# Kernel optimization log

Measured on AMD Instinct MI355X. Metric: run time of the kernel, lower is better.

The kernel has to match this reference:

```python
import jax, jax.numpy as jnp
import numpy as np
from jax import lax

B, C, W, H = 4, 64, 128, 128
K = 9            # snake kernel length
OC = 64          # out channels
EXTEND_SCOPE = 1.0
EPS = 1e-5
DN = ('NCHW', 'OIHW', 'NCHW')


def setup_inputs() -> dict:
    key = jax.random.key(0)
    ks = jax.random.split(key, 4)
    f = jax.random.normal(ks[0], (B, C, W, H), jnp.float32)
    offset_w = jax.random.normal(ks[1], (2 * K, C, 3, 3), jnp.float32) * 0.05
    offset_b = jnp.zeros((2 * K,), jnp.float32)
    bn_gamma = jnp.ones((2 * K,), jnp.float32)
    bn_beta = jnp.zeros((2 * K,), jnp.float32)
    bn_mean = jnp.zeros((2 * K,), jnp.float32)
    bn_var = jnp.ones((2 * K,), jnp.float32)
    conv_w = jax.random.normal(ks[2], (OC, C, K, 1), jnp.float32) * 0.05
    conv_b = jnp.zeros((OC,), jnp.float32)
    gn_gamma = jnp.ones((OC,), jnp.float32)
    gn_beta = jnp.zeros((OC,), jnp.float32)
    return dict(f=f, offset_w=offset_w, offset_b=offset_b, bn_gamma=bn_gamma,
                bn_beta=bn_beta, bn_mean=bn_mean, bn_var=bn_var,
                conv_w=conv_w, conv_b=conv_b, gn_gamma=gn_gamma, gn_beta=gn_beta)


def _dsconv(f, offset_w, offset_b, bn_gamma, bn_beta, bn_mean, bn_var,
            conv_w, conv_b, gn_gamma, gn_beta):
    # 1) offset branch: 3x3 conv -> BN (eval) -> tanh
    off = lax.conv_general_dilated(f, offset_w, (1, 1), 'SAME', dimension_numbers=DN)
    off = off + offset_b[None, :, None, None]
    off = (off - bn_mean[None, :, None, None]) * lax.rsqrt(bn_var + EPS)[None, :, None, None]
    off = off * bn_gamma[None, :, None, None] + bn_beta[None, :, None, None]
    off = jnp.tanh(off)
    y_off = off[:, :K]                      # [B,K,W,H]  (morph==0 uses y offsets)

    # 2) cumulative offset recurrence outward from the kernel center.
    # NOTE: indices 0 and K-1 keep their raw (non-accumulated) offsets,
    # exactly reproducing the original loop `for i in range(1, center)`.
    c = K // 2
    offs = [y_off[:, k] for k in range(K)]  # each [B,W,H]
    new = list(offs)
    new[c] = jnp.zeros_like(offs[c])
    for i in range(1, c):
        new[c + i] = new[c + i - 1] + offs[c + i]
        new[c - i] = new[c - i + 1] + offs[c - i]
    y_cum = jnp.stack(new, axis=1)          # [B,K,W,H]

    # 3) sampling coordinates (morph==0): y = row index + accumulated offset,
    # x = col index + linspace(-K//2, K//2, K) (python floor-div semantics).
    lin = jnp.linspace((-K) // 2, K // 2, K).astype(f.dtype)      # [-5..4] for K=9
    y = jnp.arange(W, dtype=f.dtype)[None, None, :, None] + y_cum * EXTEND_SCOPE
    x = jnp.broadcast_to(jnp.arange(H, dtype=f.dtype)[None, None, None, :]
                         + lin[None, :, None, None], (B, K, W, H))
    # layout [B, K*W, H] with row index = w*K + k
    ys = jnp.transpose(y, (0, 2, 1, 3)).reshape(B, K * W, H)
    xs = jnp.transpose(x, (0, 2, 1, 3)).reshape(B, K * W, H)

    # 4) bilinear gather from f (NCHW -> BWHC for channel-last gathers)
    y0 = jnp.clip(jnp.floor(ys).astype(jnp.int32), 0, W - 1)
    y1 = jnp.clip(y0 + 1, 0, W - 1)
    x0 = jnp.clip(jnp.floor(xs).astype(jnp.int32), 0, H - 1)
    x1 = jnp.clip(x0 + 1, 0, H - 1)
    fb = jnp.transpose(f, (0, 2, 3, 1))                  # [B,W,H,C]
    gather = jax.vmap(lambda fm, yy, xx: fm[yy, xx])     # -> [B,K*W,H,C]
    va0 = gather(fb, y0, x0)
    va1 = gather(fb, y0, x1)
    vb0 = gather(fb, y1, x0)
    vb1 = gather(fb, y1, x1)
    y0f, y1f = y0.astype(f.dtype), y1.astype(f.dtype)
    x0f, x1f = x0.astype(f.dtype), x1.astype(f.dtype)
    out = (va0 * ((y1f - ys) * (x1f - xs))[..., None]
           + va1 * ((y1f - ys) * (xs - x0f))[..., None]
           + vb0 * ((ys - y0f) * (x1f - xs))[..., None]
           + vb1 * ((ys - y0f) * (xs - x0f))[..., None])
    deformed = jnp.transpose(out, (0, 3, 1, 2))          # [B,C,K*W,H]

    # 5) (K,1)-strided conv collapses the K snake samples -> [B,OC,W,H]
    z = lax.conv_general_dilated(deformed, conv_w, (K, 1), 'VALID', dimension_numbers=DN)
    z = z + conv_b[None, :, None, None]

    # 6) GroupNorm(OC//4 groups) + ReLU
    G = OC // 4
    zg = z.reshape(B, G, OC // G, W, H)
    mu = zg.mean(axis=(2, 3, 4), keepdims=True)
    var = zg.var(axis=(2, 3, 4), keepdims=True)
    zg = (zg - mu) * lax.rsqrt(var + EPS)
    z = zg.reshape(B, OC, W, H) * gn_gamma[None, :, None, None] + gn_beta[None, :, None, None]
    return jax.nn.relu(z)


def reference(f, offset_w, offset_b, bn_gamma, bn_beta, bn_mean, bn_var,
              conv_w, conv_b, gn_gamma, gn_beta):
    return _dsconv(f, offset_w, offset_b, bn_gamma, bn_beta, bn_mean, bn_var,
                   conv_w, conv_b, gn_gamma, gn_beta)
```

## Files before the change

kernel.cpp:

```cpp
#include <hip/hip_runtime.h>
#include <hip/hip_bf16.h>

#define EPSV 1e-5f

typedef __attribute__((ext_vector_type(8))) short short8;
typedef __attribute__((ext_vector_type(4))) float f32x4;

__device__ __forceinline__ uint2 bilerp_pack(uint2 u00, uint2 u01, uint2 u10, uint2 u11, float4 tw) {
    float a0 = __uint_as_float(u00.x << 16) * tw.x + __uint_as_float(u01.x << 16) * tw.y
             + __uint_as_float(u10.x << 16) * tw.z + __uint_as_float(u11.x << 16) * tw.w;
    float a1 = __uint_as_float(u00.x & 0xffff0000u) * tw.x + __uint_as_float(u01.x & 0xffff0000u) * tw.y
             + __uint_as_float(u10.x & 0xffff0000u) * tw.z + __uint_as_float(u11.x & 0xffff0000u) * tw.w;
    float a2 = __uint_as_float(u00.y << 16) * tw.x + __uint_as_float(u01.y << 16) * tw.y
             + __uint_as_float(u10.y << 16) * tw.z + __uint_as_float(u11.y << 16) * tw.w;
    float a3 = __uint_as_float(u00.y & 0xffff0000u) * tw.x + __uint_as_float(u01.y & 0xffff0000u) * tw.y
             + __uint_as_float(u10.y & 0xffff0000u) * tw.z + __uint_as_float(u11.y & 0xffff0000u) * tw.w;
    uint2 pk;
    pk.x = (uint)__bfloat16_as_ushort(__float2bfloat16(a0))
         | ((uint)__bfloat16_as_ushort(__float2bfloat16(a1)) << 16);
    pk.y = (uint)__bfloat16_as_ushort(__float2bfloat16(a2))
         | ((uint)__bfloat16_as_ushort(__float2bfloat16(a3)) << 16);
    return pk;
}

__global__ __launch_bounds__(256) void k_pre(const float* __restrict__ f,
                                             const float* __restrict__ cw,
                                             const float* __restrict__ ow,
                                             ushort* __restrict__ fbh,
                                             ushort* __restrict__ flo,
                                             ushort* __restrict__ wpk,
                                             ushort* __restrict__ wpk2,
                                             float* __restrict__ stats) {
    int blk = blockIdx.x;
    int t = threadIdx.x;
    if (blk < 1024) {
        __shared__ float tile[64][65];
        int xt = blk & 1;
        int y  = (blk >> 1) & 127;
        int b  = blk >> 8;
        int x = t & 63, c0 = t >> 6;
        const float* src = f + (((size_t)b * 64) * 128 + y) * 128 + xt * 64;
#pragma unroll
        for (int i = 0; i < 64; i += 4)
            tile[c0 + i][x] = src[(size_t)(c0 + i) * 16384 + x];
        __syncthreads();
        size_t dbase = (((size_t)b * 128 + y) * 128 + xt * 64) * 64;
        int cc = t & 63, x0 = t >> 6;
#pragma unroll
        for (int i = 0; i < 64; i += 4) {
            float v = tile[cc][x0 + i];
            ushort hi = __bfloat16_as_ushort(__float2bfloat16(v));
            float vhi = __uint_as_float((uint)hi << 16);
            ushort lo = __bfloat16_as_ushort(__float2bfloat16(v - vhi));
            fbh[dbase + (size_t)(x0 + i) * 64 + cc] = hi;
            flo[dbase + (size_t)(x0 + i) * 64 + cc] = lo;
        }
    } else if (blk < 1168) {
        int idx = (blk - 1024) * 256 + t;
        int j  = idx & 7;
        int l  = (idx >> 3) & 63;
        int ot = (idx >> 9) & 3;
        int kk = (idx >> 11) & 1;
        int k  = idx >> 12;
        int c  = kk * 32 + ((l >> 4) << 3) + j;
        int oc = (ot << 4) + (l & 15);
        wpk[idx] = __bfloat16_as_ushort(__float2bfloat16(cw[((size_t)oc * 64 + c) * 9 + k]));
        if (idx < 128) stats[idx] = 0.f;
    } else {
        int idx = (blk - 1168) * 256 + t;
        int j   = idx & 7;
        int l   = (idx >> 3) & 63;
        int kk  = (idx >> 9) & 1;
        int tap = idx >> 10;
        int c   = kk * 32 + ((l >> 4) << 3) + j;
        int n   = l & 15;
        float v = (n < 9) ? ow[((size_t)n * 64 + c) * 9 + tap] : 0.f;
        ushort hi = __bfloat16_as_ushort(__float2bfloat16(v));
        float vhi = __uint_as_float((uint)hi << 16);
        ushort lo = __bfloat16_as_ushort(__float2bfloat16(v - vhi));
        wpk2[idx] = hi;
        wpk2[idx + 9216] = lo;
    }
}

__global__ __launch_bounds__(256) void k_fused(
    const ushort* __restrict__ fbh,
    const ushort* __restrict__ flo,
    const ushort* __restrict__ wpk,
    const ushort* __restrict__ wpk2,
    const float* __restrict__ ob, const float* __restrict__ bng,
    const float* __restrict__ bnb, const float* __restrict__ bnm,
    const float* __restrict__ bnv, const float* __restrict__ cb,
    float* __restrict__ z, float* __restrict__ stats)
{
    __shared__ struct {
        ushort AH[2][2048];
        ushort AL[2][2048];
        float  tup[9][32][8];
        float  cs[32][12];
    } smx;
    __shared__ float redS[16], redQ[16];

    int jb = blockIdx.x;
    int orig = (jb & 7) * 256 + (jb >> 3);
    int hq = orig & 3;
    int w  = (orig >> 2) & 127;
    int b  = orig >> 9;
    int t    = threadIdx.x;
    int lane = t & 63;
    int wid  = t >> 6;
    int m = wid & 1;
    int n = wid >> 1;

    const char* fpH = (const char*)fbh;
    const char* fpL = (const char*)flo;
    int cg  = t & 15;
    int pq  = t >> 4;
    int cgo = cg << 3;

    int frow = (m << 4) + (lane & 15);
    int frb0 = (frow << 7) + (((lane >> 4) << 4) ^ ((lane & 7) << 4));

    f32x4 acc0k = {0.f, 0.f, 0.f, 0.f};
    const short8* wp2 = (const short8*)wpk2;

    {
        int ysrc = w - 1;
        bool rok = (unsigned)ysrc < 128u;
        char* AbH = (char*)smx.AH[0];
        char* AbL = (char*)smx.AL[0];
#pragma unroll
        for (int s = 0; s < 2; ++s) {
            int px = pq + (s << 4);
            int xsrc = (hq << 5) + px - 1;
            uint2 vh = make_uint2(0u, 0u), vl = make_uint2(0u, 0u);
            if (rok && ((unsigned)xsrc < 128u)) {
                int off = ((((((b << 7) + ysrc) << 7) + xsrc)) << 7) + cgo;
                vh = *(const uint2*)(fpH + off);
                vl = *(const uint2*)(fpL + off);
            }
            int wb = (px << 7) + (cgo ^ ((px & 7) << 4));
            *(uint2*)(AbH + wb) = vh;
            *(uint2*)(AbL + wb) = vl;
        }
    }
    for (int tap = 0; tap < 9; ++tap) {
        __syncthreads();
        int cur = tap & 1;
        uint2 gh[2] = {make_uint2(0u, 0u), make_uint2(0u, 0u)};
        uint2 gl[2] = {make_uint2(0u, 0u), make_uint2(0u, 0u)};
        if (tap < 8) {
            int tn = tap + 1;
            int dy = tn / 3;
            int dx = tn - dy * 3;
            int ysrc = w + dy - 1;
            bool rok = (unsigned)ysrc < 128u;
#pragma unroll
            for (int s = 0; s < 2; ++s) {
                int px = pq + (s << 4);
                int xsrc = (hq << 5) + px + dx - 1;
                if (rok && ((unsigned)xsrc < 128u)) {
                    int off = ((((((b << 7) + ysrc) << 7) + xsrc)) << 7) + cgo;
                    gh[s] = *(const uint2*)(fpH + off);
                    gl[s] = *(const uint2*)(fpL + off);
                }
            }
        }
        if (wid < 2) {
            const char* ArH = (const char*)smx.AH[cur];
            const char* ArL = (const char*)smx.AL[cur];
            short8 ah0 = *(const short8*)(ArH + frb0);
            short8 ah1 = *(const short8*)(ArH + (frb0 ^ 64));
            short8 al0 = *(const short8*)(ArL + frb0);
            short8 al1 = *(const short8*)(ArL + (frb0 ^ 64));
            short8 wh0 = wp2[(tap * 2 + 0) * 64 + lane];
            short8 wh1 = wp2[(tap * 2 + 1) * 64 + lane];
            short8 wl0 = wp2[1152 + (tap * 2 + 0) * 64 + lane];
            short8 wl1 = wp2[1152 + (tap * 2 + 1) * 64 + lane];
            acc0k = __builtin_amdgcn_mfma_f32_16x16x32_bf16(ah0, wh0, acc0k, 0, 0, 0);
            acc0k = __builtin_amdgcn_mfma_f32_16x16x32_bf16(al0, wh0, acc0k, 0, 0, 0);
            acc0k = __builtin_amdgcn_mfma_f32_16x16x32_bf16(ah0, wl0, acc0k, 0, 0, 0);
            acc0k = __builtin_amdgcn_mfma_f32_16x16x32_bf16(ah1, wh1, acc0k, 0, 0, 0);
            acc0k = __builtin_amdgcn_mfma_f32_16x16x32_bf16(al1, wh1, acc0k, 0, 0, 0);
            acc0k = __builtin_amdgcn_mfma_f32_16x16x32_bf16(ah1, wl1, acc0k, 0, 0, 0);
        }
        if (tap < 8) {
            char* AbH = (char*)smx.AH[cur ^ 1];
            char* AbL = (char*)smx.AL[cur ^ 1];
#pragma unroll
            for (int s = 0; s < 2; ++s) {
                int px = pq + (s << 4);
                int wb = (px << 7) + (cgo ^ ((px & 7) << 4));
                *(uint2*)(AbH + wb) = gh[s];
                *(uint2*)(AbL + wb) = gl[s];
            }
        }
    }
    if (wid < 2) {
#pragma unroll
        for (int r = 0; r < 4; ++r) {
            int pxo = (m << 4) + ((lane >> 4) << 2) + r;
            int ko = lane & 15;
            if (ko < 9) smx.cs[pxo][ko] = acc0k[r];
        }
    }
    __syncthreads();
    if (t < 32) {
        float tk[9];
#pragma unroll
        for (int k = 0; k < 9; ++k) {
            float zz = smx.cs[t][k] + ob[k];
            zz = (zz - bnm[k]) * rsqrtf(bnv[k] + EPSV);
            zz = zz * bng[k] + bnb[k];
            tk[k] = tanhf(zz);
        }
        float nw_[9];
        nw_[4] = 0.f;
        nw_[5] = tk[5];
        nw_[6] = nw_[5] + tk[6];
        nw_[7] = nw_[6] + tk[7];
        nw_[8] = tk[8];
        nw_[3] = tk[3];
        nw_[2] = nw_[3] + tk[2];
        nw_[1] = nw_[2] + tk[1];
        nw_[0] = tk[0];
        int h = (hq << 5) + t;
#pragma unroll
        for (int k = 0; k < 9; ++k) {
            float ys = (float)w + nw_[k];
            float xs = (float)h + (-5.0f + 1.125f * (float)k);
            int y0 = min(max((int)floorf(ys), 0), 127);
            int y1 = min(y0 + 1, 127);
            int x0 = min(max((int)floorf(xs), 0), 127);
            int x1 = min(x0 + 1, 127);
            float wy0 = (float)y1 - ys, wy1 = ys - (float)y0;
            float wx0 = (float)x1 - xs, wx1 = xs - (float)x0;
            float* tp = smx.tup[k][t];
            tp[0] = __int_as_float(((((b << 7) + y0) << 7) + x0) << 7);
            tp[1] = __int_as_float(((((b << 7) + y0) << 7) + x1) << 7);
            tp[2] = __int_as_float(((((b << 7) + y1) << 7) + x0) << 7);
            tp[3] = __int_as_float(((((b << 7) + y1) << 7) + x1) << 7);
            tp[4] = wy0 * wx0;
            tp[5] = wy0 * wx1;
            tp[6] = wy1 * wx0;
            tp[7] = wy1 * wx1;
        }
    }
    __syncthreads();

    f32x4 acc0 = {0.f, 0.f, 0.f, 0.f};
    f32x4 acc1 = {0.f, 0.f, 0.f, 0.f};
    const short8* wp8 = (const short8*)wpk;

    {
        char* Ab = (char*)smx.AH[0];
#pragma unroll
        for (int s = 0; s < 2; ++s) {
            int px = pq + (s << 4);
            const float* tp = smx.tup[0][px];
            float4 tr = *(const float4*)tp;
            float4 tw = *(const float4*)(tp + 4);
            uint2 u00 = *(const uint2*)(fpH + __float_as_int(tr.x) + cgo);
            uint2 u01 = *(const uint2*)(fpH + __float_as_int(tr.y) + cgo);
            uint2 u10 = *(const uint2*)(fpH + __float_as_int(tr.z) + cgo);
            uint2 u11 = *(const uint2*)(fpH + __float_as_int(tr.w) + cgo);
            *(uint2*)(Ab + (px << 7) + (cgo ^ ((px & 7) << 4))) = bilerp_pack(u00, u01, u10, u11, tw);
        }
    }
    for (int k = 0; k < 9; ++k) {
        __syncthreads();
        int cur = k & 1;
        uint2 u[2][4];
        float4 twn[2];
        if (k < 8) {
#pragma unroll
            for (int s = 0; s < 2; ++s) {
                int px = pq + (s << 4);
                const float* tp = smx.tup[k + 1][px];
                float4 tr = *(const float4*)tp;
                twn[s] = *(const float4*)(tp + 4);
                u[s][0] = *(const uint2*)(fpH + __float_as_int(tr.x) + cgo);
                u[s][1] = *(const uint2*)(fpH + __float_as_int(tr.y) + cgo);
                u[s][2] = *(const uint2*)(fpH + __float_as_int(tr.z) + cgo);
                u[s][3] = *(const uint2*)(fpH + __float_as_int(tr.w) + cgo);
            }
        }
        int fb0 = (k * 8 + (n << 1)) * 64 + lane;
        short8 wf00 = wp8[fb0];
        short8 wf01 = wp8[fb0 + 64];
        short8 wf10 = wp8[fb0 + 256];
        short8 wf11 = wp8[fb0 + 320];
        const char* Ar = (const char*)smx.AH[cur];
        short8 af0 = *(const short8*)(Ar + frb0);
        short8 af1 = *(const short8*)(Ar + (frb0 ^ 64));
        acc0 = __builtin_amdgcn_mfma_f32_16x16x32_bf16(af0, wf00, acc0, 0, 0, 0);
        acc0 = __builtin_amdgcn_mfma_f32_16x16x32_bf16(af1, wf10, acc0, 0, 0, 0);
        acc1 = __builtin_amdgcn_mfma_f32_16x16x32_bf16(af0, wf01, acc1, 0, 0, 0);
        acc1 = __builtin_amdgcn_mfma_f32_16x16x32_bf16(af1, wf11, acc1, 0, 0, 0);
        if (k < 8) {
            char* Ab = (char*)smx.AH[cur ^ 1];
#pragma unroll
            for (int s = 0; s < 2; ++s) {
                int px = pq + (s << 4);
                *(uint2*)(Ab + (px << 7) + (cgo ^ ((px & 7) << 4))) =
                    bilerp_pack(u[s][0], u[s][1], u[s][2], u[s][3], twn[s]);
            }
        }
    }

    float* Z2 = (float*)&smx;
    int lane15 = lane & 15;
    float b0 = cb[(n << 5) + lane15];
    float b1 = cb[(n << 5) + 16 + lane15];
    float v00 = acc0.x + b0, v01 = acc0.y + b0, v02 = acc0.z + b0, v03 = acc0.w + b0;
    float v10 = acc1.x + b1, v11 = acc1.y + b1, v12 = acc1.z + b1, v13 = acc1.w + b1;
    float s0 = v00 + v01 + v02 + v03;
    float q0 = v00 * v00 + v01 * v01 + v02 * v02 + v03 * v03;
    float s1 = v10 + v11 + v12 + v13;
    float q1 = v10 * v10 + v11 * v11 + v12 * v12 + v13 * v13;
    if (t < 16) { redS[t] = 0.f; redQ[t] = 0.f; }
    __syncthreads();
    int g0 = (n << 3) + (lane15 >> 2);
    atomicAdd(&redS[g0], s0);     atomicAdd(&redQ[g0], q0);
    atomicAdd(&redS[g0 + 4], s1); atomicAdd(&redQ[g0 + 4], q1);
    int pxb = (m << 4) + ((lane >> 4) << 2);
    int ocb = (n << 5) + lane15;
    Z2[(pxb + 0) * 65 + ocb] = v00;
    Z2[(pxb + 1) * 65 + ocb] = v01;
    Z2[(pxb + 2) * 65 + ocb] = v02;
    Z2[(pxb + 3) * 65 + ocb] = v03;
    Z2[(pxb + 0) * 65 + ocb + 16] = v10;
    Z2[(pxb + 1) * 65 + ocb + 16] = v11;
    Z2[(pxb + 2) * 65 + ocb + 16] = v12;
    Z2[(pxb + 3) * 65 + ocb + 16] = v13;
    __syncthreads();
    if (t < 16) {
        atomicAdd(&stats[((size_t)b * 16 + t) * 2 + 0], redS[t]);
        atomicAdd(&stats[((size_t)b * 16 + t) * 2 + 1], redQ[t]);
    }
    int oc = t >> 2, part = t & 3;
    float4 o0, o1;
    o0.x = Z2[(part * 8 + 0) * 65 + oc];
    o0.y = Z2[(part * 8 + 1) * 65 + oc];
    o0.z = Z2[(part * 8 + 2) * 65 + oc];
    o0.w = Z2[(part * 8 + 3) * 65 + oc];
    o1.x = Z2[(part * 8 + 4) * 65 + oc];
    o1.y = Z2[(part * 8 + 5) * 65 + oc];
    o1.z = Z2[(part * 8 + 6) * 65 + oc];
    o1.w = Z2[(part * 8 + 7) * 65 + oc];
    float* zp = z + (((size_t)(b << 6) + oc) << 14) + (w << 7) + (hq << 5) + part * 8;
    *(float4*)zp = o0;
    *(float4*)(zp + 4) = o1;
}

__global__ __launch_bounds__(256) void k_gn(const float* __restrict__ z,
                                            const float* __restrict__ stats,
                                            const float* __restrict__ gg,
                                            const float* __restrict__ gb,
                                            float* __restrict__ out) {
    int idx = blockIdx.x * 256 + threadIdx.x;
    size_t base = (size_t)idx * 4;
    int oc = (int)((base >> 14) & 63);
    int b  = (int)(base >> 20);
    int g  = oc >> 2;
    float sm = stats[((size_t)b * 16 + g) * 2 + 0];
    float sq = stats[((size_t)b * 16 + g) * 2 + 1];
    const float cnt = 65536.f;
    float mu  = sm / cnt;
    float var = sq / cnt - mu * mu;
    float inv = rsqrtf(var + EPSV);
    float gam = gg[oc] * inv;
    float bet = gb[oc] - mu * gam;
    float4 v = *(const float4*)(z + base);
    v.x = fmaxf(v.x * gam + bet, 0.f);
    v.y = fmaxf(v.y * gam + bet, 0.f);
    v.z = fmaxf(v.z * gam + bet, 0.f);
    v.w = fmaxf(v.w * gam + bet, 0.f);
    *(float4*)(out + base) = v;
}

extern "C" void kernel_launch(void* const* d_in, const int* in_sizes, int n_in,
                              void* d_out, int out_size, void* d_ws, size_t ws_size,
                              hipStream_t stream) {
    const float* f   = (const float*)d_in[0];
    const float* ow  = (const float*)d_in[1];
    const float* ob  = (const float*)d_in[2];
    const float* bng = (const float*)d_in[3];
    const float* bnb = (const float*)d_in[4];
    const float* bnm = (const float*)d_in[5];
    const float* bnv = (const float*)d_in[6];
    const float* cw  = (const float*)d_in[7];
    const float* cb  = (const float*)d_in[8];
    const float* gg  = (const float*)d_in[9];
    const float* gb  = (const float*)d_in[10];

    char* wsb = (char*)d_ws;
    ushort* fbh  = (ushort*)wsb;
    ushort* flo  = (ushort*)(wsb + 8388608);
    ushort* wpk  = (ushort*)(wsb + 16777216);
    ushort* wpk2 = (ushort*)(wsb + 16850944);
    float*  z    = (float*)(wsb + 16887808);
    float*  st   = (float*)(wsb + 33665024);

    k_pre<<<1204, 256, 0, stream>>>(f, cw, ow, fbh, flo, wpk, wpk2, st);
    k_fused<<<2048, 256, 0, stream>>>(fbh, flo, wpk, wpk2, ob, bng, bnb, bnm, bnv, cb, z, st);
    k_gn<<<4096, 256, 0, stream>>>(z, st, gg, gb, (float*)d_out);
}
```

Baseline: 158.2 us.

## Stage a 9-row bf16 input window in LDS via direct global-to-LDS loads

The fused kernel now preloads a 9-row by 42-column bf16 window of the input for each block into shared memory using global_load_lds, overlapping the load with the offset-conv MFMA pass. The deformable bilinear samples are then gathered from LDS instead of global memory, and the per-tap double-buffered staging loops with their barriers are removed. The intermediate z tensor is also stored as bf16, with k_gn reading eight values per thread, which halves the intermediate traffic at some precision cost. This trades a much larger LDS footprint for fewer scattered global gathers, and occupancy is capped at three blocks per CU.

```diff
diff --git a/kernel.cpp b/kernel.cpp
--- a/kernel.cpp
+++ b/kernel.cpp
@@ -6,21 +6,26 @@
 typedef __attribute__((ext_vector_type(8))) short short8;
 typedef __attribute__((ext_vector_type(4))) float f32x4;
 
-__device__ __forceinline__ uint2 bilerp_pack(uint2 u00, uint2 u01, uint2 u10, uint2 u11, float4 tw) {
-    float a0 = __uint_as_float(u00.x << 16) * tw.x + __uint_as_float(u01.x << 16) * tw.y
-             + __uint_as_float(u10.x << 16) * tw.z + __uint_as_float(u11.x << 16) * tw.w;
-    float a1 = __uint_as_float(u00.x & 0xffff0000u) * tw.x + __uint_as_float(u01.x & 0xffff0000u) * tw.y
-             + __uint_as_float(u10.x & 0xffff0000u) * tw.z + __uint_as_float(u11.x & 0xffff0000u) * tw.w;
-    float a2 = __uint_as_float(u00.y << 16) * tw.x + __uint_as_float(u01.y << 16) * tw.y
-             + __uint_as_float(u10.y << 16) * tw.z + __uint_as_float(u11.y << 16) * tw.w;
-    float a3 = __uint_as_float(u00.y & 0xffff0000u) * tw.x + __uint_as_float(u01.y & 0xffff0000u) * tw.y
-             + __uint_as_float(u10.y & 0xffff0000u) * tw.z + __uint_as_float(u11.y & 0xffff0000u) * tw.w;
-    uint2 pk;
-    pk.x = (uint)__bfloat16_as_ushort(__float2bfloat16(a0))
-         | ((uint)__bfloat16_as_ushort(__float2bfloat16(a1)) << 16);
-    pk.y = (uint)__bfloat16_as_ushort(__float2bfloat16(a2))
-         | ((uint)__bfloat16_as_ushort(__float2bfloat16(a3)) << 16);
-    return pk;
+__device__ __forceinline__ void gl_lds16(const void* g, void* l) {
+    __builtin_amdgcn_global_load_lds(
+        (const __attribute__((address_space(1))) unsigned int*)g,
+        (__attribute__((address_space(3))) unsigned int*)l, 16, 0, 0);
+}
+
+__device__ __forceinline__ unsigned int bl2(unsigned int a, unsigned int b,
+                                            unsigned int c, unsigned int d,
+                                            float w00, float w01, float w10, float w11) {
+    float lo = __uint_as_float(a << 16) * w00 + __uint_as_float(b << 16) * w01
+             + __uint_as_float(c << 16) * w10 + __uint_as_float(d << 16) * w11;
+    float hi = __uint_as_float(a & 0xffff0000u) * w00 + __uint_as_float(b & 0xffff0000u) * w01
+             + __uint_as_float(c & 0xffff0000u) * w10 + __uint_as_float(d & 0xffff0000u) * w11;
+    return ((unsigned int)__bfloat16_as_ushort(__float2bfloat16(lo)))
+         | (((unsigned int)__bfloat16_as_ushort(__float2bfloat16(hi))) << 16);
+}
+
+__device__ __forceinline__ unsigned int pk2(float a, float b) {
+    return ((unsigned int)__bfloat16_as_ushort(__float2bfloat16(a)))
+         | (((unsigned int)__bfloat16_as_ushort(__float2bfloat16(b))) << 16);
 }
 
 __global__ __launch_bounds__(256) void k_pre(const float* __restrict__ f,
@@ -50,7 +55,7 @@
         for (int i = 0; i < 64; i += 4) {
             float v = tile[cc][x0 + i];
             ushort hi = __bfloat16_as_ushort(__float2bfloat16(v));
-            float vhi = __uint_as_float((uint)hi << 16);
+            float vhi = __uint_as_float((unsigned int)hi << 16);
             ushort lo = __bfloat16_as_ushort(__float2bfloat16(v - vhi));
             fbh[dbase + (size_t)(x0 + i) * 64 + cc] = hi;
             flo[dbase + (size_t)(x0 + i) * 64 + cc] = lo;
@@ -76,14 +81,14 @@
         int n   = l & 15;
         float v = (n < 9) ? ow[((size_t)n * 64 + c) * 9 + tap] : 0.f;
         ushort hi = __bfloat16_as_ushort(__float2bfloat16(v));
-        float vhi = __uint_as_float((uint)hi << 16);
+        float vhi = __uint_as_float((unsigned int)hi << 16);
         ushort lo = __bfloat16_as_ushort(__float2bfloat16(v - vhi));
         wpk2[idx] = hi;
         wpk2[idx + 9216] = lo;
     }
 }
 
-__global__ __launch_bounds__(256) void k_fused(
+__global__ __launch_bounds__(256, 3) void k_fused(
     const ushort* __restrict__ fbh,
     const ushort* __restrict__ flo,
     const ushort* __restrict__ wpk,
@@ -91,14 +96,15 @@
     const float* __restrict__ ob, const float* __restrict__ bng,
     const float* __restrict__ bnb, const float* __restrict__ bnm,
     const float* __restrict__ bnv, const float* __restrict__ cb,
-    float* __restrict__ z, float* __restrict__ stats)
+    ushort* __restrict__ z, float* __restrict__ stats)
 {
-    __shared__ struct {
-        ushort AH[2][2048];
-        ushort AL[2][2048];
-        float  tup[9][32][8];
-        float  cs[32][12];
-    } smx;
+    __shared__ union {
+        struct {
+            ushort win[24192];
+            float  tup[9][32][4];
+        } p;
+        float Z2[32 * 65];
+    } sm;
     __shared__ float redS[16], redQ[16];
 
     int jb = blockIdx.x;
@@ -106,110 +112,88 @@
     int hq = orig & 3;
     int w  = (orig >> 2) & 127;
     int b  = orig >> 9;
+    int h0 = hq << 5;
     int t    = threadIdx.x;
     int lane = t & 63;
     int wid  = t >> 6;
     int m = wid & 1;
     int n = wid >> 1;
-
-    const char* fpH = (const char*)fbh;
-    const char* fpL = (const char*)flo;
-    int cg  = t & 15;
-    int pq  = t >> 4;
-    int cgo = cg << 3;
-
-    int frow = (m << 4) + (lane & 15);
-    int frb0 = (frow << 7) + (((lane >> 4) << 4) ^ ((lane & 7) << 4));
-
-    f32x4 acc0k = {0.f, 0.f, 0.f, 0.f};
-    const short8* wp2 = (const short8*)wpk2;
-
-    {
-        int ysrc = w - 1;
-        bool rok = (unsigned)ysrc < 128u;
-        char* AbH = (char*)smx.AH[0];
-        char* AbL = (char*)smx.AL[0];
-#pragma unroll
-        for (int s = 0; s < 2; ++s) {
-            int px = pq + (s << 4);
-            int xsrc = (hq << 5) + px - 1;
-            uint2 vh = make_uint2(0u, 0u), vl = make_uint2(0u, 0u);
-            if (rok && ((unsigned)xsrc < 128u)) {
-                int off = ((((((b << 7) + ysrc) << 7) + xsrc)) << 7) + cgo;
-                vh = *(const uint2*)(fpH + off);
-                vl = *(const uint2*)(fpL + off);
+    const char* winb = (const char*)sm.p.win;
+
+#pragma unroll
+    for (int p = 0; p < 12; ++p) {
+        if (p == 11 && t >= 208) break;
+        int ib = p * 4096 + t * 16;
+        int ri = ib / 5376;
+        int wb = ib - ri * 5376;
+        int dys = ri < 3 ? ri + 3 : (ri < 6 ? ri - 3 : ri);
+        int grow = min(max(w + dys - 4, 0), 127);
+        int colIdx = wb >> 7;
+        int c16 = (wb >> 4) & 7;
+        int gcol = min(max(h0 - 5 + colIdx, 0), 127);
+        int sch = c16 ^ (colIdx & 7);
+        const ushort* src = fbh + ((((size_t)b << 7) + grow) * 128 + gcol) * 64 + (sch << 3);
+        gl_lds16(src, (void*)(winb + ib));
+    }
+    asm volatile("s_waitcnt vmcnt(8)" ::: "memory");
+    __builtin_amdgcn_sched_barrier(0);
+    __syncthreads();
+
+    if (wid < 2) {
+        f32x4 acck = {0.f, 0.f, 0.f, 0.f};
+        const short8* wp2 = (const short8*)wpk2;
+        int px0 = (m << 4) + (lane & 15);
+        int q = lane >> 4;
+#pragma unroll
+        for (int tap = 0; tap < 9; ++tap) {
+            int dy = tap / 3, dx = tap - dy * 3;
+            int ysrc = w + dy - 1;
+            if ((unsigned)ysrc < 128u) {
+                int col = h0 + px0 + dx - 1;
+                bool ok = (unsigned)col < 128u;
+                int xslot = px0 + dx + 4;
+                int rbase = dy * 5376 + (xslot << 7);
+                uint4 h0v = *(const uint4*)(winb + rbase + ((q ^ (xslot & 7)) << 4));
+                uint4 h1v = *(const uint4*)(winb + rbase + (((q + 4) ^ (xslot & 7)) << 4));
+                int colc = min(max(col, 0), 127);
+                const ushort* lsrc = flo + ((((size_t)b << 7) + ysrc) * 128 + colc) * 64 + (q << 3);
+                uint4 l0v = *(const uint4*)lsrc;
+                uint4 l1v = *(const uint4*)(lsrc + 32);
+                if (!ok) {
+                    h0v = make_uint4(0, 0, 0, 0); h1v = make_uint4(0, 0, 0, 0);
+                    l0v = make_uint4(0, 0, 0, 0); l1v = make_uint4(0, 0, 0, 0);
+                }
+                short8 wh0 = wp2[(tap * 2 + 0) * 64 + lane];
+                short8 wh1 = wp2[(tap * 2 + 1) * 64 + lane];
+                short8 wl0 = wp2[1152 + (tap * 2 + 0) * 64 + lane];
+                short8 wl1 = wp2[1152 + (tap * 2 + 1) * 64 + lane];
+                short8 ah0 = *(short8*)&h0v, ah1 = *(short8*)&h1v;
+                short8 al0 = *(short8*)&l0v, al1 = *(short8*)&l1v;
+                acck = __builtin_amdgcn_mfma_f32_16x16x32_bf16(ah0, wh0, acck, 0, 0, 0);
+                acck = __builtin_amdgcn_mfma_f32_16x16x32_bf16(al0, wh0, acck, 0, 0, 0);
+                acck = __builtin_amdgcn_mfma_f32_16x16x32_bf16(ah0, wl0, acck, 0, 0, 0);
+                acck = __builtin_amdgcn_mfma_f32_16x16x32_bf16(ah1, wh1, acck, 0, 0, 0);
+                acck = __builtin_amdgcn_mfma_f32_16x16x32_bf16(al1, wh1, acck, 0, 0, 0);
+                acck = __builtin_amdgcn_mfma_f32_16x16x32_bf16(ah1, wl1, acck, 0, 0, 0);
             }
-            int wb = (px << 7) + (cgo ^ ((px & 7) << 4));
-            *(uint2*)(AbH + wb) = vh;
-            *(uint2*)(AbL + wb) = vl;
-        }
-    }
-    for (int tap = 0; tap < 9; ++tap) {
-        __syncthreads();
-        int cur = tap & 1;
-        uint2 gh[2] = {make_uint2(0u, 0u), make_uint2(0u, 0u)};
-        uint2 gl[2] = {make_uint2(0u, 0u), make_uint2(0u, 0u)};
-        if (tap < 8) {
-            int tn = tap + 1;
-            int dy = tn / 3;
-            int dx = tn - dy * 3;
-            int ysrc = w + dy - 1;
-            bool rok = (unsigned)ysrc < 128u;
-#pragma unroll
-            for (int s = 0; s < 2; ++s) {
-                int px = pq + (s << 4);
-                int xsrc = (hq << 5) + px + dx - 1;
-                if (rok && ((unsigned)xsrc < 128u)) {
-                    int off = ((((((b << 7) + ysrc) << 7) + xsrc)) << 7) + cgo;
-                    gh[s] = *(const uint2*)(fpH + off);
-                    gl[s] = *(const uint2*)(fpL + off);
-                }
-            }
-        }
-        if (wid < 2) {
-            const char* ArH = (const char*)smx.AH[cur];
-            const char* ArL = (const char*)smx.AL[cur];
-            short8 ah0 = *(const short8*)(ArH + frb0);
-            short8 ah1 = *(const short8*)(ArH + (frb0 ^ 64));
-            short8 al0 = *(const short8*)(ArL + frb0);
-            short8 al1 = *(const short8*)(ArL + (frb0 ^ 64));
-            short8 wh0 = wp2[(tap * 2 + 0) * 64 + lane];
-            short8 wh1 = wp2[(tap * 2 + 1) * 64 + lane];
-            short8 wl0 = wp2[1152 + (tap * 2 + 0) * 64 + lane];
-            short8 wl1 = wp2[1152 + (tap * 2 + 1) * 64 + lane];
-            acc0k = __builtin_amdgcn_mfma_f32_16x16x32_bf16(ah0, wh0, acc0k, 0, 0, 0);
-            acc0k = __builtin_amdgcn_mfma_f32_16x16x32_bf16(al0, wh0, acc0k, 0, 0, 0);
-            acc0k = __builtin_amdgcn_mfma_f32_16x16x32_bf16(ah0, wl0, acc0k, 0, 0, 0);
-            acc0k = __builtin_amdgcn_mfma_f32_16x16x32_bf16(ah1, wh1, acc0k, 0, 0, 0);
-            acc0k = __builtin_amdgcn_mfma_f32_16x16x32_bf16(al1, wh1, acc0k, 0, 0, 0);
-            acc0k = __builtin_amdgcn_mfma_f32_16x16x32_bf16(ah1, wl1, acc0k, 0, 0, 0);
-        }
-        if (tap < 8) {
-            char* AbH = (char*)smx.AH[cur ^ 1];
-            char* AbL = (char*)smx.AL[cur ^ 1];
-#pragma unroll
-            for (int s = 0; s < 2; ++s) {
-                int px = pq + (s << 4);
-                int wb = (px << 7) + (cgo ^ ((px & 7) << 4));
-                *(uint2*)(AbH + wb) = gh[s];
-                *(uint2*)(AbL + wb) = gl[s];
-            }
-        }
-    }
-    if (wid < 2) {
+        }
+        float* csm = (float*)sm.p.tup;
 #pragma unroll
         for (int r = 0; r < 4; ++r) {
             int pxo = (m << 4) + ((lane >> 4) << 2) + r;
             int ko = lane & 15;
-            if (ko < 9) smx.cs[pxo][ko] = acc0k[r];
-        }
-    }
-    __syncthreads();
+            if (ko < 9) csm[pxo * 9 + ko] = acck[r];
+        }
+    }
+    asm volatile("s_waitcnt vmcnt(0)" ::: "memory");
+    __syncthreads();
+
     if (t < 32) {
+        const float* csm = (const float*)sm.p.tup;
         float tk[9];
 #pragma unroll
         for (int k = 0; k < 9; ++k) {
-            float zz = smx.cs[t][k] + ob[k];
+            float zz = csm[t * 9 + k] + ob[k];
             zz = (zz - bnm[k]) * rsqrtf(bnv[k] + EPSV);
             zz = zz * bng[k] + bnb[k];
             tk[k] = tanhf(zz);
@@ -224,26 +208,21 @@
         nw_[2] = nw_[3] + tk[2];
         nw_[1] = nw_[2] + tk[1];
         nw_[0] = tk[0];
-        int h = (hq << 5) + t;
 #pragma unroll
         for (int k = 0; k < 9; ++k) {
             float ys = (float)w + nw_[k];
-            float xs = (float)h + (-5.0f + 1.125f * (float)k);
             int y0 = min(max((int)floorf(ys), 0), 127);
             int y1 = min(y0 + 1, 127);
-            int x0 = min(max((int)floorf(xs), 0), 127);
-            int x1 = min(x0 + 1, 127);
             float wy0 = (float)y1 - ys, wy1 = ys - (float)y0;
-            float wx0 = (float)x1 - xs, wx1 = xs - (float)x0;
-            float* tp = smx.tup[k][t];
-            tp[0] = __int_as_float(((((b << 7) + y0) << 7) + x0) << 7);
-            tp[1] = __int_as_float(((((b << 7) + y0) << 7) + x1) << 7);
-            tp[2] = __int_as_float(((((b << 7) + y1) << 7) + x0) << 7);
-            tp[3] = __int_as_float(((((b << 7) + y1) << 7) + x1) << 7);
-            tp[4] = wy0 * wx0;
-            tp[5] = wy0 * wx1;
-            tp[6] = wy1 * wx0;
-            tp[7] = wy1 * wx1;
+            int d0 = min(max(y0 - w + 4, 0), 8);
+            int d1 = min(max(y1 - w + 4, 0), 8);
+            int p0 = d0 < 3 ? d0 + 3 : (d0 < 6 ? d0 - 3 : d0);
+            int p1 = d1 < 3 ? d1 + 3 : (d1 < 6 ? d1 - 3 : d1);
+            float4 tv;
+            tv.x = wy0; tv.y = wy1;
+            tv.z = __int_as_float(p0 * 5376);
+            tv.w = __int_as_float(p1 * 5376);
+            *(float4*)sm.p.tup[k][t] = tv;
         }
     }
     __syncthreads();
@@ -251,64 +230,53 @@
     f32x4 acc0 = {0.f, 0.f, 0.f, 0.f};
     f32x4 acc1 = {0.f, 0.f, 0.f, 0.f};
     const short8* wp8 = (const short8*)wpk;
-
-    {
-        char* Ab = (char*)smx.AH[0];
-#pragma unroll
-        for (int s = 0; s < 2; ++s) {
-            int px = pq + (s << 4);
-            const float* tp = smx.tup[0][px];
-            float4 tr = *(const float4*)tp;
-            float4 tw = *(const float4*)(tp + 4);
-            uint2 u00 = *(const uint2*)(fpH + __float_as_int(tr.x) + cgo);
-            uint2 u01 = *(const uint2*)(fpH + __float_as_int(tr.y) + cgo);
-            uint2 u10 = *(const uint2*)(fpH + __float_as_int(tr.z) + cgo);
-            uint2 u11 = *(const uint2*)(fpH + __float_as_int(tr.w) + cgo);
-            *(uint2*)(Ab + (px << 7) + (cgo ^ ((px & 7) << 4))) = bilerp_pack(u00, u01, u10, u11, tw);
-        }
-    }
+    int px = (lane & 15) + (m << 4);
+    int q  = lane >> 4;
+    float fpx = (float)(h0 + px);
+#pragma unroll 3
     for (int k = 0; k < 9; ++k) {
-        __syncthreads();
-        int cur = k & 1;
-        uint2 u[2][4];
-        float4 twn[2];
-        if (k < 8) {
-#pragma unroll
-            for (int s = 0; s < 2; ++s) {
-                int px = pq + (s << 4);
-                const float* tp = smx.tup[k + 1][px];
-                float4 tr = *(const float4*)tp;
-                twn[s] = *(const float4*)(tp + 4);
-                u[s][0] = *(const uint2*)(fpH + __float_as_int(tr.x) + cgo);
-                u[s][1] = *(const uint2*)(fpH + __float_as_int(tr.y) + cgo);
-                u[s][2] = *(const uint2*)(fpH + __float_as_int(tr.z) + cgo);
-                u[s][3] = *(const uint2*)(fpH + __float_as_int(tr.w) + cgo);
-            }
-        }
+        float4 tv = *(const float4*)sm.p.tup[k][px];
+        float xs = fpx + (-5.0f + 1.125f * (float)k);
+        int x0 = min(max((int)floorf(xs), 0), 127);
+        int x1 = min(x0 + 1, 127);
+        float wx0 = (float)x1 - xs;
+        float wx1 = xs - (float)x0;
+        float w00 = tv.x * wx0, w01 = tv.x * wx1, w10 = tv.y * wx0, w11 = tv.y * wx1;
+        int rb0 = __float_as_int(tv.z), rb1 = __float_as_int(tv.w);
+        int cx0 = x0 - h0 + 5, cx1 = x1 - h0 + 5;
+        int s00 = rb0 + (cx0 << 7), s01 = rb0 + (cx1 << 7);
+        int s10 = rb1 + (cx0 << 7), s11 = rb1 + (cx1 << 7);
+        int qa0 = (q ^ (cx0 & 7)) << 4,       qa1 = (q ^ (cx1 & 7)) << 4;
+        int qb0 = ((q + 4) ^ (cx0 & 7)) << 4, qb1 = ((q + 4) ^ (cx1 & 7)) << 4;
+        uint4 a00 = *(const uint4*)(winb + s00 + qa0);
+        uint4 a01 = *(const uint4*)(winb + s01 + qa1);
+        uint4 a10 = *(const uint4*)(winb + s10 + qa0);
+        uint4 a11 = *(const uint4*)(winb + s11 + qa1);
+        uint4 b00 = *(const uint4*)(winb + s00 + qb0);
+        uint4 b01 = *(const uint4*)(winb + s01 + qb1);
+        uint4 b10 = *(const uint4*)(winb + s10 + qb0);
+        uint4 b11 = *(const uint4*)(winb + s11 + qb1);
+        uint4 f0u, f1u;
+        f0u.x = bl2(a00.x, a01.x, a10.x, a11.x, w00, w01, w10, w11);
+        f0u.y = bl2(a00.y, a01.y, a10.y, a11.y, w00, w01, w10, w11);
+        f0u.z = bl2(a00.z, a01.z, a10.z, a11.z, w00, w01, w10, w11);
+        f0u.w = bl2(a00.w, a01.w, a10.w, a11.w, w00, w01, w10, w11);
+        f1u.x = bl2(b00.x, b01.x, b10.x, b11.x, w00, w01, w10, w11);
+        f1u.y = bl2(b00.y, b01.y, b10.y, b11.y, w00, w01, w10, w11);
+        f1u.z = bl2(b00.z, b01.z, b10.z, b11.z, w00, w01, w10, w11);
+        f1u.w = bl2(b00.w, b01.w, b10.w, b11.w, w00, w01, w10, w11);
+        short8 af0 = *(short8*)&f0u, af1 = *(short8*)&f1u;
         int fb0 = (k * 8 + (n << 1)) * 64 + lane;
         short8 wf00 = wp8[fb0];
         short8 wf01 = wp8[fb0 + 64];
         short8 wf10 = wp8[fb0 + 256];
         short8 wf11 = wp8[fb0 + 320];
-        const char* Ar = (const char*)smx.AH[cur];
-        short8 af0 = *(const short8*)(Ar + frb0);
-        short8 af1 = *(const short8*)(Ar + (frb0 ^ 64));
         acc0 = __builtin_amdgcn_mfma_f32_16x16x32_bf16(af0, wf00, acc0, 0, 0, 0);
         acc0 = __builtin_amdgcn_mfma_f32_16x16x32_bf16(af1, wf10, acc0, 0, 0, 0);
         acc1 = __builtin_amdgcn_mfma_f32_16x16x32_bf16(af0, wf01, acc1, 0, 0, 0);
         acc1 = __builtin_amdgcn_mfma_f32_16x16x32_bf16(af1, wf11, acc1, 0, 0, 0);
-        if (k < 8) {
-            char* Ab = (char*)smx.AH[cur ^ 1];
-#pragma unroll
-            for (int s = 0; s < 2; ++s) {
-                int px = pq + (s << 4);
-                *(uint2*)(Ab + (px << 7) + (cgo ^ ((px & 7) << 4))) =
-                    bilerp_pack(u[s][0], u[s][1], u[s][2], u[s][3], twn[s]);
-            }
-        }
-    }
-
-    float* Z2 = (float*)&smx;
+    }
+
     int lane15 = lane & 15;
     float b0 = cb[(n << 5) + lane15];
     float b1 = cb[(n << 5) + 16 + lane15];
@@ -320,6 +288,7 @@
     float q1 = v10 * v10 + v11 * v11 + v12 * v12 + v13 * v13;
     if (t < 16) { redS[t] = 0.f; redQ[t] = 0.f; }
     __syncthreads();
+    float* Z2 = (float*)&sm;
     int g0 = (n << 3) + (lane15 >> 2);
     atomicAdd(&redS[g0], s0);     atomicAdd(&redQ[g0], q0);
     atomicAdd(&redS[g0 + 4], s1); atomicAdd(&redQ[g0 + 4], q1);
@@ -339,27 +308,30 @@
         atomicAdd(&stats[((size_t)b * 16 + t) * 2 + 1], redQ[t]);
     }
     int oc = t >> 2, part = t & 3;
-    float4 o0, o1;
-    o0.x = Z2[(part * 8 + 0) * 65 + oc];
-    o0.y = Z2[(part * 8 + 1) * 65 + oc];
-    o0.z = Z2[(part * 8 + 2) * 65 + oc];
-    o0.w = Z2[(part * 8 + 3) * 65 + oc];
-    o1.x = Z2[(part * 8 + 4) * 65 + oc];
-    o1.y = Z2[(part * 8 + 5) * 65 + oc];
-    o1.z = Z2[(part * 8 + 6) * 65 + oc];
-    o1.w = Z2[(part * 8 + 7) * 65 + oc];
-    float* zp = z + (((size_t)(b << 6) + oc) << 14) + (w << 7) + (hq << 5) + part * 8;
-    *(float4*)zp = o0;
-    *(float4*)(zp + 4) = o1;
-}
-
-__global__ __launch_bounds__(256) void k_gn(const float* __restrict__ z,
+    float o0x = Z2[(part * 8 + 0) * 65 + oc];
+    float o0y = Z2[(part * 8 + 1) * 65 + oc];
+    float o0z = Z2[(part * 8 + 2) * 65 + oc];
+    float o0w = Z2[(part * 8 + 3) * 65 + oc];
+    float o1x = Z2[(part * 8 + 4) * 65 + oc];
+    float o1y = Z2[(part * 8 + 5) * 65 + oc];
+    float o1z = Z2[(part * 8 + 6) * 65 + oc];
+    float o1w = Z2[(part * 8 + 7) * 65 + oc];
+    uint4 pk;
+    pk.x = pk2(o0x, o0y);
+    pk.y = pk2(o0z, o0w);
+    pk.z = pk2(o1x, o1y);
+    pk.w = pk2(o1z, o1w);
+    ushort* zp = z + (((size_t)(b << 6) + oc) << 14) + (w << 7) + (hq << 5) + part * 8;
+    *(uint4*)zp = pk;
+}
+
+__global__ __launch_bounds__(256) void k_gn(const ushort* __restrict__ z,
                                             const float* __restrict__ stats,
                                             const float* __restrict__ gg,
                                             const float* __restrict__ gb,
                                             float* __restrict__ out) {
     int idx = blockIdx.x * 256 + threadIdx.x;
-    size_t base = (size_t)idx * 4;
+    size_t base = (size_t)idx * 8;
     int oc = (int)((base >> 14) & 63);
     int b  = (int)(base >> 20);
     int g  = oc >> 2;
@@ -371,12 +343,18 @@
     float inv = rsqrtf(var + EPSV);
     float gam = gg[oc] * inv;
     float bet = gb[oc] - mu * gam;
-    float4 v = *(const float4*)(z + base);
-    v.x = fmaxf(v.x * gam + bet, 0.f);
-    v.y = fmaxf(v.y * gam + bet, 0.f);
-    v.z = fmaxf(v.z * gam + bet, 0.f);
-    v.w = fmaxf(v.w * gam + bet, 0.f);
-    *(float4*)(out + base) = v;
+    uint4 v = *(const uint4*)(z + base);
+    float4 o0, o1;
+    o0.x = fmaxf(__uint_as_float(v.x << 16) * gam + bet, 0.f);
+    o0.y = fmaxf(__uint_as_float(v.x & 0xffff0000u) * gam + bet, 0.f);
+    o0.z = fmaxf(__uint_as_float(v.y << 16) * gam + bet, 0.f);
+    o0.w = fmaxf(__uint_as_float(v.y & 0xffff0000u) * gam + bet, 0.f);
+    o1.x = fmaxf(__uint_as_float(v.z << 16) * gam + bet, 0.f);
+    o1.y = fmaxf(__uint_as_float(v.z & 0xffff0000u) * gam + bet, 0.f);
+    o1.z = fmaxf(__uint_as_float(v.w << 16) * gam + bet, 0.f);
+    o1.w = fmaxf(__uint_as_float(v.w & 0xffff0000u) * gam + bet, 0.f);
+    *(float4*)(out + base) = o0;
+    *(float4*)(out + base + 4) = o1;
 }
 
 extern "C" void kernel_launch(void* const* d_in, const int* in_sizes, int n_in,
@@ -399,10 +377,10 @@
     ushort* flo  = (ushort*)(wsb + 8388608);
     ushort* wpk  = (ushort*)(wsb + 16777216);
     ushort* wpk2 = (ushort*)(wsb + 16850944);
-    float*  z    = (float*)(wsb + 16887808);
-    float*  st   = (float*)(wsb + 33665024);
+    ushort* z    = (ushort*)(wsb + 16887808);
+    float*  st   = (float*)(wsb + 25276416);
 
     k_pre<<<1204, 256, 0, stream>>>(f, cw, ow, fbh, flo, wpk, wpk2, st);
     k_fused<<<2048, 256, 0, stream>>>(fbh, flo, wpk, wpk2, ob, bng, bnb, bnm, bnv, cb, z, st);
-    k_gn<<<4096, 256, 0, stream>>>(z, st, gg, gb, (float*)d_out);
-}
+    k_gn<<<2048, 256, 0, stream>>>(z, st, gg, gb, (float*)d_out);
+}
```

After: 162.9 us. +2.9%, slower.
